# Performance work log

Measured on AMD Instinct MI355X. Metric: run time of the kernel, lower is better.

The kernel has to match this reference:

```python
import jax, jax.numpy as jnp
import numpy as np

N = 100000        # nodes
E = 1600000       # edges (before self-loops)
IN = 128          # in_dim
HID = 16          # hidden_dim per head
HEADS = 8
OUT = 40          # out_dim (classes)
BN_EPS = 1e-5
NEG_SLOPE = 0.2


def setup_inputs() -> dict:
    key = jax.random.key(0)
    ks = jax.random.split(key, 16)
    s = 0.05
    return {
        "x": jax.random.normal(ks[0], (N, IN), dtype=jnp.float32),
        "edge_index": jax.random.randint(ks[1], (2, E), 0, N, dtype=jnp.int64),
        "W1": jax.random.normal(ks[2], (IN, HEADS * HID), dtype=jnp.float32) * s,
        "att_src1": jax.random.normal(ks[3], (HEADS, HID), dtype=jnp.float32) * s,
        "att_dst1": jax.random.normal(ks[4], (HEADS, HID), dtype=jnp.float32) * s,
        "bias1": jax.random.normal(ks[5], (HEADS * HID,), dtype=jnp.float32) * s,
        "bn_gamma": 1.0 + jax.random.normal(ks[6], (HEADS * HID,), dtype=jnp.float32) * 0.1,
        "bn_beta": jax.random.normal(ks[7], (HEADS * HID,), dtype=jnp.float32) * 0.1,
        "bn_mean": jax.random.normal(ks[8], (HEADS * HID,), dtype=jnp.float32) * 0.1,
        "bn_var": jax.random.uniform(ks[9], (HEADS * HID,), dtype=jnp.float32, minval=0.5, maxval=1.5),
        "W2": jax.random.normal(ks[10], (HEADS * HID, OUT), dtype=jnp.float32) * s,
        "att_src2": jax.random.normal(ks[11], (1, OUT), dtype=jnp.float32) * s,
        "att_dst2": jax.random.normal(ks[12], (1, OUT), dtype=jnp.float32) * s,
        "bias2": jax.random.normal(ks[13], (OUT,), dtype=jnp.float32) * s,
        "W_skip": jax.random.normal(ks[14], (IN, HEADS * HID), dtype=jnp.float32) * s,
        "b_skip": jax.random.normal(ks[15], (HEADS * HID,), dtype=jnp.float32) * s,
    }


def gat_conv(x, src, dst, W, a_src, a_dst, bias, heads, ch, concat):
    """PyG GATConv (eval mode): per-edge attention, segment softmax over dst, scatter-add."""
    n = x.shape[0]
    h = (x @ W).reshape(n, heads, ch)                      # [N,H,C]
    alpha_s = jnp.einsum("nhc,hc->nh", h, a_src)            # [N,H]
    alpha_d = jnp.einsum("nhc,hc->nh", h, a_dst)            # [N,H]
    e = jax.nn.leaky_relu(alpha_s[src] + alpha_d[dst], NEG_SLOPE)   # [E,H]
    # numerically stable segment softmax over destination node
    m = jax.ops.segment_max(e, dst, num_segments=n)          # [N,H]
    ex = jnp.exp(e - m[dst])                                 # [E,H]
    denom = jax.ops.segment_sum(ex, dst, num_segments=n)     # [N,H]
    alpha = ex / (denom[dst] + 1e-16)                        # [E,H]
    out = jax.ops.segment_sum(alpha[:, :, None] * h[src], dst, num_segments=n)  # [N,H,C]
    out = out.reshape(n, heads * ch) if concat else out.mean(axis=1)
    return out + bias


def reference(x, edge_index, W1, att_src1, att_dst1, bias1,
              bn_gamma, bn_beta, bn_mean, bn_var,
              W2, att_src2, att_dst2, bias2, W_skip, b_skip):
    n = x.shape[0]
    # add self-loops (PyG GATConv default)
    loops = jnp.arange(n, dtype=edge_index.dtype)
    src = jnp.concatenate([edge_index[0], loops])
    dst = jnp.concatenate([edge_index[1], loops])

    identity = x @ W_skip + b_skip                           # skip projection

    h = gat_conv(x, src, dst, W1, att_src1, att_dst1, bias1, HEADS, HID, True)
    h = (h - bn_mean) * (bn_gamma / jnp.sqrt(bn_var + BN_EPS)) + bn_beta  # BN eval
    h = jax.nn.elu(h)                                        # dropout: eval no-op
    h = h + identity

    att_s2 = att_src2  # [1,OUT] heads=1
    out = gat_conv(h, src, dst, W2, att_s2, att_dst2, bias2, 1, OUT, False)
    return jax.nn.log_softmax(out, axis=1)
```

## Files before the change

kernel.cpp:

```cpp
#include <hip/hip_runtime.h>
#include <math.h>

#define NEG_SLOPE 0.2f
#define BN_EPS 1e-5f
#define BSH 9
#define BMASK 511
#define LOG2E 1.44269504088896f
#define BCAP 12288
#define CH_MAX 3400

typedef __attribute__((ext_vector_type(8))) short short8;
typedef __attribute__((ext_vector_type(4))) float f32x4;
typedef __attribute__((ext_vector_type(2))) float f32x2;

__device__ __forceinline__ float wave_max64(float v) {
  #pragma unroll
  for (int o = 32; o; o >>= 1) v = fmaxf(v, __shfl_xor(v, o, 64));
  return v;
}
__device__ __forceinline__ float wave_sum64(float v) {
  #pragma unroll
  for (int o = 32; o; o >>= 1) v += __shfl_xor(v, o, 64);
  return v;
}

__device__ __forceinline__ unsigned pack2bf(float a, float b) {
  unsigned ua = __float_as_uint(a);
  unsigned ub = __float_as_uint(b);
  ua = ua + 0x7fffu + ((ua >> 16) & 1u);
  ub = ub + 0x7fffu + ((ub >> 16) & 1u);
  return (ua >> 16) | (ub & 0xffff0000u);
}
__device__ __forceinline__ float bf_lo(unsigned u) { return __uint_as_float(u << 16); }
__device__ __forceinline__ float bf_hi(unsigned u) { return __uint_as_float(u & 0xffff0000u); }

union U8 { short8 s; uint4 u; };

__global__ void prep_kernel(const float* __restrict__ W1,
                            const float* __restrict__ att_s,
                            const float* __restrict__ att_d,
                            float* __restrict__ Mext,
                            const float* __restrict__ W2,
                            const float* __restrict__ att_s2,
                            const float* __restrict__ att_d2,
                            float* __restrict__ M2ext,
                            int* __restrict__ bcur, int NB)
{
  int k = threadIdx.x;
  if (k < NB) bcur[k] = 0;
  if (k >= 128) return;
  #pragma unroll
  for (int h = 0; h < 8; ++h) {
    float s = 0.f, d = 0.f;
    #pragma unroll
    for (int c = 0; c < 16; ++c) {
      float w = W1[k * 128 + h * 16 + c];
      s += w * att_s[h * 16 + c];
      d += w * att_d[h * 16 + c];
    }
    Mext[k * 16 + h] = s * LOG2E;
    Mext[k * 16 + 8 + h] = d * LOG2E;
  }
  float s2 = 0.f, d2 = 0.f;
  #pragma unroll
  for (int c = 0; c < 40; ++c) {
    float w = W2[k * 40 + c];
    s2 += w * att_s2[c];
    d2 += w * att_d2[c];
  }
  M2ext[k * 2] = s2 * LOG2E;
  M2ext[k * 2 + 1] = d2 * LOG2E;
}

__global__ __launch_bounds__(256) void gemm1_scatter_kernel(
    const float* __restrict__ X, const float* __restrict__ W1,
    const float* __restrict__ Wsk, const float* __restrict__ bsk,
    const float* __restrict__ Mext,
    unsigned short* __restrict__ h1f8, unsigned* __restrict__ identb,
    float* __restrict__ alpha_s, float* __restrict__ alpha_d, int N,
    const int* __restrict__ esrc, const int* __restrict__ edst,
    int* __restrict__ bcur, unsigned* __restrict__ pkbuf,
    int E, int T, int chunk, int NB, int G1)
{
  __shared__ uint4 Asm4[2048];
  const int t = threadIdx.x;

  if ((int)blockIdx.x >= G1) {
    int* hist  = (int*)Asm4;
    int* lbase = hist + 256;
    int* lcur  = hist + 512;
    unsigned* spk = (unsigned*)(hist + 768);
    unsigned char* sbk = (unsigned char*)(spk + CH_MAX);
    const int bid = (int)blockIdx.x - G1;
    hist[t] = 0;
    __syncthreads();
    int s0 = bid * chunk;
    int s1 = min(s0 + chunk, T);
    for (int i = s0 + t; i < s1; i += 256) {
      int d, s;
      if (i < E) { d = edst[i]; s = esrc[i]; } else { d = s = i - E; }
      int b = d >> BSH;
      int li = i - s0;
      spk[li] = ((unsigned)(d & BMASK) << 17) | (unsigned)s;
      sbk[li] = (unsigned char)b;
      atomicAdd(&hist[b], 1);
    }
    __syncthreads();
    if (t < NB) {
      int h = hist[t];
      lbase[t] = t * BCAP + (h ? atomicAdd(&bcur[t], h) : 0);
      lcur[t] = 0;
    }
    __syncthreads();
    const int cnt2 = s1 - s0;
    for (int li = t; li < cnt2; li += 256) {
      int b = sbk[li];
      int p = lbase[b] + atomicAdd(&lcur[b], 1);
      pkbuf[p] = spk[li];
    }
    return;
  }

  const int l = t & 63, wave = t >> 6;
  const int lx = l & 15, ly = l >> 4;
  const int row0 = blockIdx.x * 128;
  const int wn0 = wave * 64;

  short8 b[4][4];
  short8 b4[4] = {};
  #pragma unroll
  for (int nf = 0; nf < 4; ++nf) {
    int c = wn0 + nf * 16 + lx;
    const float* bp = (c < 128) ? (W1 + c) : (Wsk + c - 128);
    #pragma unroll
    for (int kf = 0; kf < 4; ++kf) {
      int k0 = kf * 32 + ly * 8;
      U8 f;
      f.u.x = pack2bf(bp[(k0 + 0) * 128], bp[(k0 + 1) * 128]);
      f.u.y = pack2bf(bp[(k0 + 2) * 128], bp[(k0 + 3) * 128]);
      f.u.z = pack2bf(bp[(k0 + 4) * 128], bp[(k0 + 5) * 128]);
      f.u.w = pack2bf(bp[(k0 + 6) * 128], bp[(k0 + 7) * 128]);
      b[nf][kf] = f.s;
    }
  }
  if (wave == 0) {
    const float* bp = Mext + lx;
    #pragma unroll
    for (int kf = 0; kf < 4; ++kf) {
      int k0 = kf * 32 + ly * 8;
      U8 f;
      f.u.x = pack2bf(bp[(k0 + 0) * 16], bp[(k0 + 1) * 16]);
      f.u.y = pack2bf(bp[(k0 + 2) * 16], bp[(k0 + 3) * 16]);
      f.u.z = pack2bf(bp[(k0 + 4) * 16], bp[(k0 + 5) * 16]);
      f.u.w = pack2bf(bp[(k0 + 6) * 16], bp[(k0 + 7) * 16]);
      b4[kf] = f.s;
    }
  }

  {
    int rl = t >> 1;
    int half = t & 1;
    int r = row0 + rl;
    const float* xp = X + (size_t)r * 128 + half * 64;
    #pragma unroll
    for (int i = 0; i < 8; ++i) {
      float4 f0 = make_float4(0.f, 0.f, 0.f, 0.f), f1 = f0;
      if (r < N) {
        f0 = *(const float4*)(xp + i * 8);
        f1 = *(const float4*)(xp + i * 8 + 4);
      }
      uint4 u;
      u.x = pack2bf(f0.x, f0.y); u.y = pack2bf(f0.z, f0.w);
      u.z = pack2bf(f1.x, f1.y); u.w = pack2bf(f1.z, f1.w);
      int woff = (rl * 256 + half * 128 + i * 16) ^ ((rl & 7) << 4);
      *(uint4*)((char*)Asm4 + woff) = u;
    }
  }
  __syncthreads();

  float bval[4];
  if (wave >= 2) {
    #pragma unroll
    for (int nf = 0; nf < 4; ++nf) bval[nf] = bsk[(wave - 2) * 64 + nf * 16 + lx];
  }

  for (int mf = 0; mf < 8; ++mf) {
    short8 a[4];
    int rowl = mf * 16 + lx;
    #pragma unroll
    for (int kf = 0; kf < 4; ++kf)
      a[kf] = *(short8*)((char*)Asm4 + ((rowl * 256 + kf * 64 + ly * 16) ^ ((lx & 7) << 4)));

    int rbase = row0 + mf * 16 + ly * 4;

    #pragma unroll
    for (int nf = 0; nf < 4; ++nf) {
      f32x4 acc = {0.f, 0.f, 0.f, 0.f};
      #pragma unroll
      for (int kf = 0; kf < 4; ++kf)
        acc = __builtin_amdgcn_mfma_f32_16x16x32_bf16(a[kf], b[nf][kf], acc, 0, 0, 0);
      if (wave < 2) {
        int c = wn0 + nf * 16 + lx;
        #pragma unroll
        for (int reg = 0; reg < 4; ++reg) {
          float v = acc[reg];
          float vp = __shfl_xor(v, 1, 64);
          int r = rbase + reg;
          if (!(lx & 1) && r < N) {
            int u = __builtin_amdgcn_cvt_pk_fp8_f32(v, vp, 0, false);
            *(unsigned short*)((char*)h1f8 + (unsigned)r * 128u + (unsigned)c) =
                (unsigned short)u;
          }
        }
      } else {
        int c = (wave - 2) * 64 + nf * 16 + lx;
        #pragma unroll
        for (int reg = 0; reg < 4; ++reg) {
          float v = acc[reg] + bval[nf];
          float vp = __shfl_xor(v, 1, 64);
          int r = rbase + reg;
          if (!(lx & 1) && r < N)
            identb[(unsigned)r * 64u + (unsigned)(c >> 1)] = pack2bf(v, vp);
        }
      }
    }

    if (wave == 0) {
      f32x4 acc = {0.f, 0.f, 0.f, 0.f};
      #pragma unroll
      for (int kf = 0; kf < 4; ++kf)
        acc = __builtin_amdgcn_mfma_f32_16x16x32_bf16(a[kf], b4[kf], acc, 0, 0, 0);
      #pragma unroll
      for (int reg = 0; reg < 4; ++reg) {
        int r = rbase + reg;
        if (r < N) {
          if (lx < 8) alpha_s[(size_t)r * 8 + lx] = acc[reg];
          else        alpha_d[(size_t)r * 8 + (lx - 8)] = acc[reg];
        }
      }
    }
  }
}

__global__ __launch_bounds__(256) void passB_kernel(
    const unsigned* __restrict__ pkbuf, const int* __restrict__ bcnt,
    int* __restrict__ starts, int* __restrict__ ends,
    int* __restrict__ ssrc, int N)
{
  __shared__ int cnt[512];
  __shared__ int ps[256];
  __shared__ int cur[512];
  const int t = threadIdx.x;
  const int b = blockIdx.x;
  const int bs = b * BCAP;
  const int be = bs + bcnt[b];

  cnt[t] = 0; cnt[t + 256] = 0;
  __syncthreads();
  for (int i = bs + t; i < be; i += 256)
    atomicAdd(&cnt[pkbuf[i] >> 17], 1);
  __syncthreads();

  int a = cnt[2 * t], b2 = cnt[2 * t + 1];
  ps[t] = a + b2;
  __syncthreads();
  for (int d = 1; d < 256; d <<= 1) {
    int u = (t >= d) ? ps[t - d] : 0;
    __syncthreads();
    ps[t] += u;
    __syncthreads();
  }
  int excl = ps[t] - (a + b2);
  cur[2 * t] = excl;
  cur[2 * t + 1] = excl + a;
  __syncthreads();

  const int node0 = b << BSH;
  {
    int n0 = node0 + 2 * t, n1 = node0 + 2 * t + 1;
    if (n0 < N) { starts[n0] = bs + cur[2 * t];     ends[n0] = bs + cur[2 * t] + a; }
    if (n1 < N) { starts[n1] = bs + cur[2 * t + 1]; ends[n1] = bs + cur[2 * t + 1] + b2; }
  }
  __syncthreads();

  for (int i = bs + t; i < be; i += 256) {
    unsigned pk = pkbuf[i];
    int d = pk >> 17;
    int p = atomicAdd(&cur[d], 1);
    ssrc[bs + p] = (int)(pk & 0x1FFFFu);
  }
}

__global__ __launch_bounds__(256) void agg1_kernel(
    const int* __restrict__ starts, const int* __restrict__ ends,
    const int* __restrict__ ssrc,
    const float* __restrict__ as1, const float* __restrict__ ad1,
    const unsigned short* __restrict__ h1f8,
    const float* __restrict__ bias1, const float* __restrict__ gamma,
    const float* __restrict__ beta, const float* __restrict__ mean,
    const float* __restrict__ var,
    const unsigned* __restrict__ identb, unsigned* __restrict__ hpostb, int N)
{
  const int w = threadIdx.x >> 6, l = threadIdx.x & 63;
  const int n = blockIdx.x * 4 + w;
  if (n >= N) return;
  const int e8 = l & 7;
  const int hh = l >> 3;
  const int hb4 = (l & 56) << 2;
  const int c0 = l * 2;
  const unsigned l2 = (unsigned)(l * 2);
  const float adp = ad1[(unsigned)n * 8u + (unsigned)hh];
  const int jb = starts[n], je = ends[n];

  const float bb0 = bias1[c0], bb1 = bias1[c0 + 1];
  const float sc0 = gamma[c0] * rsqrtf(var[c0] + BN_EPS);
  const float sc1 = gamma[c0 + 1] * rsqrtf(var[c0 + 1] + BN_EPS);
  const float mn0 = mean[c0], mn1 = mean[c0 + 1];
  const float bt0 = beta[c0], bt1 = beta[c0 + 1];

  const char* h1c = (const char*)h1f8;

  float dsum = 0.f;
  f32x2 acc2 = {0.f, 0.f};

#define PHASE2(K, SVEC, EW) { \
    unsigned sk = (unsigned)__builtin_amdgcn_readlane(SVEC, (K)); \
    float ewk = __uint_as_float((unsigned) \
        __builtin_amdgcn_ds_swizzle((int)__float_as_uint(EW), 0x18 | ((K) << 5))); \
    unsigned u8 = *(const unsigned short*)(h1c + ((size_t)sk << 7) + l2); \
    f32x2 hv = __builtin_amdgcn_cvt_pk_f32_fp8((int)u8, false); \
    acc2 += ewk * hv; }

  int j = jb;
  for (; j + 8 <= je; j += 8) {
    int svec = ssrc[j + e8];
    float e = as1[(unsigned)svec * 8u + (unsigned)hh] + adp;
    e = fmaxf(e, NEG_SLOPE * e);
    float ew = exp2f(e);
    dsum += ew;
    PHASE2(0, svec, ew) PHASE2(1, svec, ew) PHASE2(2, svec, ew) PHASE2(3, svec, ew)
    PHASE2(4, svec, ew) PHASE2(5, svec, ew) PHASE2(6, svec, ew) PHASE2(7, svec, ew)
  }
  int rem = je - j;
  if (rem > 0) {
    int jj = j + (e8 < rem ? e8 : 0);
    int svec = ssrc[jj];
    float e = as1[(unsigned)svec * 8u + (unsigned)hh] + adp;
    e = fmaxf(e, NEG_SLOPE * e);
    float ew = (e8 < rem) ? exp2f(e) : 0.f;
    dsum += ew;
    for (int k = 0; k < rem; ++k) {
      unsigned sk = (unsigned)__builtin_amdgcn_readlane(svec, k);
      float ewk = __uint_as_float(
          __builtin_amdgcn_ds_bpermute(hb4 + (k << 2), __float_as_uint(ew)));
      unsigned u8 = *(const unsigned short*)(h1c + ((size_t)sk << 7) + l2);
      f32x2 hv = __builtin_amdgcn_cvt_pk_f32_fp8((int)u8, false);
      acc2 += ewk * hv;
    }
  }
#undef PHASE2

  dsum += __shfl_xor(dsum, 1, 64);
  dsum += __shfl_xor(dsum, 2, 64);
  dsum += __shfl_xor(dsum, 4, 64);

  float inv = 1.f / (dsum + 1e-16f);
  unsigned uid = identb[(unsigned)n * 64u + (unsigned)l];
  float o0 = acc2.x * inv + bb0;
  float o1 = acc2.y * inv + bb1;
  o0 = (o0 - mn0) * sc0 + bt0;
  o1 = (o1 - mn1) * sc1 + bt1;
  o0 = o0 > 0.f ? o0 : expm1f(o0);
  o1 = o1 > 0.f ? o1 : expm1f(o1);
  o0 += bf_lo(uid); o1 += bf_hi(uid);
  hpostb[(unsigned)n * 64u + (unsigned)l] = pack2bf(o0, o1);
}

__global__ __launch_bounds__(256) void gemm2_kernel(
    const unsigned* __restrict__ hpostb, const float* __restrict__ W2,
    const float* __restrict__ M2ext,
    unsigned* __restrict__ h2a8, unsigned* __restrict__ h2b28,
    float* __restrict__ as2, float* __restrict__ ad2, int N)
{
  const int t = threadIdx.x;
  const int l = t & 63, wave = t >> 6;
  const int lx = l & 15, ly = l >> 4;
  const int row0 = blockIdx.x * 128;

  short8 b[3][4];
  short8 b4[4];
  {
    #pragma unroll
    for (int nf = 0; nf < 3; ++nf) {
      int col = nf * 16 + lx;
      bool v = col < 40;
      const float* bp = W2 + (v ? col : 0);
      #pragma unroll
      for (int kf = 0; kf < 4; ++kf) {
        int k0 = kf * 32 + ly * 8;
        U8 f;
        if (v) {
          f.u.x = pack2bf(bp[(k0 + 0) * 40], bp[(k0 + 1) * 40]);
          f.u.y = pack2bf(bp[(k0 + 2) * 40], bp[(k0 + 3) * 40]);
          f.u.z = pack2bf(bp[(k0 + 4) * 40], bp[(k0 + 5) * 40]);
          f.u.w = pack2bf(bp[(k0 + 6) * 40], bp[(k0 + 7) * 40]);
        } else {
          f.u = make_uint4(0, 0, 0, 0);
        }
        b[nf][kf] = f.s;
      }
    }
    bool va = lx < 2;
    const float* bp = M2ext + (va ? lx : 0);
    #pragma unroll
    for (int kf = 0; kf < 4; ++kf) {
      int k0 = kf * 32 + ly * 8;
      U8 f;
      if (va) {
        f.u.x = pack2bf(bp[(k0 + 0) * 2], bp[(k0 + 1) * 2]);
        f.u.y = pack2bf(bp[(k0 + 2) * 2], bp[(k0 + 3) * 2]);
        f.u.z = pack2bf(bp[(k0 + 4) * 2], bp[(k0 + 5) * 2]);
        f.u.w = pack2bf(bp[(k0 + 6) * 2], bp[(k0 + 7) * 2]);
      } else {
        f.u = make_uint4(0, 0, 0, 0);
      }
      b4[kf] = f.s;
    }
  }

  #pragma unroll
  for (int i2 = 0; i2 < 2; ++i2) {
    int mf = wave * 2 + i2;
    int arow = row0 + mf * 16 + lx;
    short8 a[4];
    #pragma unroll
    for (int kf = 0; kf < 4; ++kf) {
      U8 f;
      f.u = make_uint4(0, 0, 0, 0);
      if (arow < N)
        f.u = *(const uint4*)(hpostb + (unsigned)arow * 64u + (unsigned)(kf * 16 + ly * 4));
      a[kf] = f.s;
    }

    int rbase = row0 + mf * 16 + ly * 4;

    #pragma unroll
    for (int nf = 0; nf < 3; ++nf) {
      f32x4 acc = {0.f, 0.f, 0.f, 0.f};
      #pragma unroll
      for (int kf = 0; kf < 4; ++kf)
        acc = __builtin_amdgcn_mfma_f32_16x16x32_bf16(a[kf], b[nf][kf], acc, 0, 0, 0);
      int c = nf * 16 + lx;
      #pragma unroll
      for (int reg = 0; reg < 4; ++reg) {
        float v = acc[reg];
        float v1 = __shfl_xor(v, 1, 64);
        float v2 = __shfl_xor(v, 2, 64);
        float v3 = __shfl_xor(v1, 2, 64);
        int r = rbase + reg;
        if (r < N && c < 40 && !(lx & 3)) {
          int u = __builtin_amdgcn_cvt_pk_fp8_f32(v, v1, 0, false);
          u = __builtin_amdgcn_cvt_pk_fp8_f32(v2, v3, u, true);
          int c4 = c >> 2;
          if (c < 32) h2a8[((unsigned)r << 3) + (unsigned)c4] = (unsigned)u;
          else        h2b28[((unsigned)r << 1) + (unsigned)(c4 - 8)] = (unsigned)u;
        }
      }
    }
    {
      f32x4 acc = {0.f, 0.f, 0.f, 0.f};
      #pragma unroll
      for (int kf = 0; kf < 4; ++kf)
        acc = __builtin_amdgcn_mfma_f32_16x16x32_bf16(a[kf], b4[kf], acc, 0, 0, 0);
      #pragma unroll
      for (int reg = 0; reg < 4; ++reg) {
        int r = rbase + reg;
        if (r < N) {
          if (lx == 0) as2[r] = acc[reg];
          else if (lx == 1) ad2[r] = acc[reg];
        }
      }
    }
  }
}

__global__ __launch_bounds__(256) void agg2_kernel(
    const int* __restrict__ starts, const int* __restrict__ ends,
    const int* __restrict__ ssrc,
    const float* __restrict__ as2, const float* __restrict__ ad2,
    const unsigned* __restrict__ h2a8, const unsigned* __restrict__ h2b28,
    const float* __restrict__ bias2,
    float* __restrict__ outp, int N)
{
  const int w = threadIdx.x >> 6, l = threadIdx.x & 63;
  const int n = blockIdx.x * 4 + w;
  if (n >= N) return;
  const int g = l / 10;
  const int q = l - g * 10;
  const bool act = l < 60;
  const float ad = ad2[n];
  const int jb = starts[n], je = ends[n];

  const char* hbase = (q < 8) ? ((const char*)h2a8 + (unsigned)q * 4u)
                              : ((const char*)h2b28 + (unsigned)(q - 8) * 4u);
  const unsigned hshift = (q < 8) ? 5u : 3u;
  const char* as2c = (const char*)as2;

  float dsum = 0.f;
  f32x2 acc01 = {0.f, 0.f}, acc23 = {0.f, 0.f};

#define EDGE2(JJ, GUARD) { \
    bool v_ = act && (GUARD); \
    unsigned s = v_ ? (unsigned)ssrc[JJ] : 0u; \
    float e = *(const float*)(as2c + (s << 2)) + ad; \
    e = fmaxf(e, NEG_SLOPE * e); \
    float ex = v_ ? exp2f(e) : 0.f; \
    unsigned u = *(const unsigned*)(hbase + ((size_t)s << hshift)); \
    dsum += ex; \
    f32x2 lo = __builtin_amdgcn_cvt_pk_f32_fp8((int)u, false); \
    f32x2 hi = __builtin_amdgcn_cvt_pk_f32_fp8((int)u, true); \
    acc01 += ex * lo; \
    acc23 += ex * hi; }

  int j = jb;
  for (; j + 12 <= je; j += 12) {
    EDGE2(j + g, true)
    EDGE2(j + 6 + g, true)
  }
  for (; j < je; j += 6) {
    EDGE2(j + g, (j + g) < je)
  }
#undef EDGE2

  float a0 = acc01.x, a1 = acc01.y, a2 = acc23.x, a3 = acc23.y;

#define COMB(A) { \
    float t_ = A + __shfl(A, l + 30, 64); \
    A = t_ + __shfl(t_, l + 10, 64) + __shfl(t_, l + 20, 64); }
  COMB(a0) COMB(a1) COMB(a2) COMB(a3) COMB(dsum)
#undef COMB

  float inv = 1.f / (dsum + 1e-16f);
  float o0 = a0 * inv + bias2[q * 4 + 0];
  float o1 = a1 * inv + bias2[q * 4 + 1];
  float o2 = a2 * inv + bias2[q * 4 + 2];
  float o3 = a3 * inv + bias2[q * 4 + 3];

  float m4 = fmaxf(fmaxf(o0, o1), fmaxf(o2, o3));
  float mx = wave_max64(l < 10 ? m4 : -3.4e38f);
  float se = wave_sum64(l < 10 ? __expf(o0 - mx) + __expf(o1 - mx) +
                                 __expf(o2 - mx) + __expf(o3 - mx) : 0.f);
  float ls = logf(se);
  if (l < 10)
    *(float4*)&outp[(size_t)n * 40 + q * 4] =
        make_float4(o0 - mx - ls, o1 - mx - ls, o2 - mx - ls, o3 - mx - ls);
}

extern "C" void kernel_launch(void* const* d_in, const int* in_sizes, int n_in,
                              void* d_out, int out_size, void* d_ws, size_t ws_size,
                              hipStream_t stream)
{
  const float* x        = (const float*)d_in[0];
  const int*   ei       = (const int*)d_in[1];
  const float* W1       = (const float*)d_in[2];
  const float* att_src1 = (const float*)d_in[3];
  const float* att_dst1 = (const float*)d_in[4];
  const float* bias1    = (const float*)d_in[5];
  const float* bn_gamma = (const float*)d_in[6];
  const float* bn_beta  = (const float*)d_in[7];
  const float* bn_mean  = (const float*)d_in[8];
  const float* bn_var   = (const float*)d_in[9];
  const float* W2       = (const float*)d_in[10];
  const float* att_src2 = (const float*)d_in[11];
  const float* att_dst2 = (const float*)d_in[12];
  const float* bias2    = (const float*)d_in[13];
  const float* W_skip   = (const float*)d_in[14];
  const float* b_skip   = (const float*)d_in[15];

  const int N = in_sizes[0] / 128;
  const int E = in_sizes[1] / 2;
  const int T = E + N;
  const int NB = (N + BMASK) >> BSH;

  char* p = (char*)d_ws;
  auto alloc = [&](size_t bytes) { char* q = p; p += (bytes + 255) & ~255ull; return q; };
  unsigned short* h1f8 = (unsigned short*)alloc((size_t)N * 128);
  unsigned* hpostb = (unsigned*)alloc((size_t)N * 64 * 4);
  unsigned* identb = (unsigned*)alloc((size_t)N * 64 * 4);
  float* as1     = (float*)alloc((size_t)N * 8 * 4);
  float* ad1     = (float*)alloc((size_t)N * 8 * 4);
  float* Mext    = (float*)alloc(128 * 16 * 4);
  float* M2ext   = (float*)alloc(128 * 2 * 4);
  int*   starts  = (int*)alloc((size_t)N * 4);
  int*   ends    = (int*)alloc((size_t)N * 4);
  unsigned* pkbuf= (unsigned*)alloc((size_t)NB * BCAP * 4);
  int*   ssrc    = (int*)alloc((size_t)NB * BCAP * 4);
  int*   bcur    = (int*)alloc((size_t)NB * 4);
  unsigned* h2a8  = (unsigned*)h1f8;
  unsigned* h2b28 = (unsigned*)((char*)h1f8 + (size_t)N * 32);
  float* as2 = as1;
  float* ad2 = ad1;

  const int* ei_src = ei;
  const int* ei_dst = ei + E;

  prep_kernel<<<1, 256, 0, stream>>>(W1, att_src1, att_dst1, Mext,
                                     W2, att_src2, att_dst2, M2ext,
                                     bcur, NB);

  const int G1 = (N + 127) / 128;
  int NBLK_A = (T + CH_MAX - 1) / CH_MAX;
  if (NBLK_A < 512) NBLK_A = 512;
  const int chunk = (T + NBLK_A - 1) / NBLK_A;
  gemm1_scatter_kernel<<<G1 + NBLK_A, 256, 0, stream>>>(
      x, W1, W_skip, b_skip, Mext, h1f8, identb, as1, ad1, N,
      ei_src, ei_dst, bcur, pkbuf, E, T, chunk, NB, G1);

  passB_kernel<<<NB, 256, 0, stream>>>(pkbuf, bcur, starts, ends, ssrc, N);

  agg1_kernel<<<(N + 3) / 4, 256, 0, stream>>>(starts, ends, ssrc, as1, ad1, h1f8,
                                               bias1, bn_gamma, bn_beta, bn_mean, bn_var,
                                               identb, hpostb, N);
  gemm2_kernel<<<(N + 127) / 128, 256, 0, stream>>>(hpostb, W2, M2ext,
                                                    h2a8, h2b28, as2, ad2, N);
  agg2_kernel<<<(N + 3) / 4, 256, 0, stream>>>(starts, ends, ssrc, as2, ad2,
                                               h2a8, h2b28, bias2,
                                               (float*)d_out, N);
}
```

Before: 230.3 us.

## Prepack bf16 weight fragments in prep kernel and store skip projection as fp8

The prep kernel now runs on four blocks and packs W1/W_skip, the attention projection matrices and W2 into bf16 column-major buffers. The GEMM kernels can then load MFMA B fragments with single 16-byte loads instead of strided fp32 gathers and per-block conversion. The skip projection identity is also stored as fp8 instead of bf16, which halves its write and read traffic between gemm1 and agg1. The cost is lower precision on the residual term.

```diff
diff --git a/kernel.cpp b/kernel.cpp
--- a/kernel.cpp
+++ b/kernel.cpp
@@ -36,47 +36,87 @@
 
 union U8 { short8 s; uint4 u; };
 
-__global__ void prep_kernel(const float* __restrict__ W1,
-                            const float* __restrict__ att_s,
-                            const float* __restrict__ att_d,
-                            float* __restrict__ Mext,
-                            const float* __restrict__ W2,
-                            const float* __restrict__ att_s2,
-                            const float* __restrict__ att_d2,
-                            float* __restrict__ M2ext,
-                            int* __restrict__ bcur, int NB)
+__global__ __launch_bounds__(256) void prep_kernel(
+    const float* __restrict__ W1, const float* __restrict__ Wsk,
+    const float* __restrict__ att_s, const float* __restrict__ att_d,
+    const float* __restrict__ W2,
+    const float* __restrict__ att_s2, const float* __restrict__ att_d2,
+    unsigned short* __restrict__ Bbuf, unsigned short* __restrict__ Mextbuf,
+    unsigned short* __restrict__ B2buf,
+    int* __restrict__ bcur, int NB)
 {
-  int k = threadIdx.x;
-  if (k < NB) bcur[k] = 0;
-  if (k >= 128) return;
-  #pragma unroll
-  for (int h = 0; h < 8; ++h) {
-    float s = 0.f, d = 0.f;
-    #pragma unroll
-    for (int c = 0; c < 16; ++c) {
-      float w = W1[k * 128 + h * 16 + c];
-      s += w * att_s[h * 16 + c];
-      d += w * att_d[h * 16 + c];
-    }
-    Mext[k * 16 + h] = s * LOG2E;
-    Mext[k * 16 + 8 + h] = d * LOG2E;
-  }
-  float s2 = 0.f, d2 = 0.f;
-  #pragma unroll
-  for (int c = 0; c < 40; ++c) {
-    float w = W2[k * 40 + c];
-    s2 += w * att_s2[c];
-    d2 += w * att_d2[c];
-  }
-  M2ext[k * 2] = s2 * LOG2E;
-  M2ext[k * 2 + 1] = d2 * LOG2E;
+  const int t = threadIdx.x;
+  const int bid = blockIdx.x;
+
+  if (bid == 0) {
+    __shared__ float Ms[128][16];
+    __shared__ float M2s[128][2];
+    if (t < NB) bcur[t] = 0;
+    if (t < 128) {
+      int k = t;
+      #pragma unroll
+      for (int h = 0; h < 8; ++h) {
+        float s = 0.f, d = 0.f;
+        #pragma unroll
+        for (int c = 0; c < 16; ++c) {
+          float w = W1[k * 128 + h * 16 + c];
+          s += w * att_s[h * 16 + c];
+          d += w * att_d[h * 16 + c];
+        }
+        Ms[k][h] = s * LOG2E;
+        Ms[k][8 + h] = d * LOG2E;
+      }
+      float s2 = 0.f, d2 = 0.f;
+      #pragma unroll
+      for (int c = 0; c < 40; ++c) {
+        float w = W2[k * 40 + c];
+        s2 += w * att_s2[c];
+        d2 += w * att_d2[c];
+      }
+      M2s[k][0] = s2 * LOG2E;
+      M2s[k][1] = d2 * LOG2E;
+    }
+    __syncthreads();
+    unsigned* Mu = (unsigned*)Mextbuf;
+    for (int idx = t; idx < 16 * 64; idx += 256) {
+      int h = idx >> 6, u = idx & 63;
+      Mu[h * 64 + u] = pack2bf(Ms[2 * u][h], Ms[2 * u + 1][h]);
+    }
+    unsigned* B2u = (unsigned*)B2buf;
+    for (int idx = t; idx < 2 * 64; idx += 256) {
+      int cc = idx >> 6, u = idx & 63;
+      B2u[(48 + cc) * 64 + u] = pack2bf(M2s[2 * u][cc], M2s[2 * u + 1][cc]);
+    }
+  } else if (bid <= 2) {
+    int c = (bid - 1) * 128 + (t >> 1);
+    int half = t & 1;
+    const float* src = (c < 128) ? (W1 + c) : (Wsk + (c - 128));
+    unsigned* out = (unsigned*)Bbuf + c * 64 + half * 32;
+    #pragma unroll 8
+    for (int u = 0; u < 32; ++u) {
+      int k = half * 64 + 2 * u;
+      out[u] = pack2bf(src[(size_t)k * 128], src[(size_t)(k + 1) * 128]);
+    }
+  } else {
+    unsigned* B2u = (unsigned*)B2buf;
+    for (int idx = t; idx < 40 * 64; idx += 256) {
+      int c = idx >> 6, u = idx & 63;
+      B2u[c * 64 + u] = pack2bf(W2[(2 * u) * 40 + c], W2[(2 * u + 1) * 40 + c]);
+    }
+    for (int idx = t; idx < 22 * 64; idx += 256) {
+      int zc = idx >> 6, u = idx & 63;
+      int c = (zc < 8) ? (40 + zc) : (50 + (zc - 8));
+      B2u[c * 64 + u] = 0;
+    }
+  }
 }
 
 __global__ __launch_bounds__(256) void gemm1_scatter_kernel(
-    const float* __restrict__ X, const float* __restrict__ W1,
-    const float* __restrict__ Wsk, const float* __restrict__ bsk,
-    const float* __restrict__ Mext,
-    unsigned short* __restrict__ h1f8, unsigned* __restrict__ identb,
+    const float* __restrict__ X,
+    const unsigned short* __restrict__ Bbuf,
+    const unsigned short* __restrict__ Mextbuf,
+    const float* __restrict__ bsk,
+    unsigned short* __restrict__ h1f8, unsigned short* __restrict__ identf8,
     float* __restrict__ alpha_s, float* __restrict__ alpha_d, int N,
     const int* __restrict__ esrc, const int* __restrict__ edst,
     int* __restrict__ bcur, unsigned* __restrict__ pkbuf,
@@ -131,30 +171,14 @@
   #pragma unroll
   for (int nf = 0; nf < 4; ++nf) {
     int c = wn0 + nf * 16 + lx;
-    const float* bp = (c < 128) ? (W1 + c) : (Wsk + c - 128);
-    #pragma unroll
-    for (int kf = 0; kf < 4; ++kf) {
-      int k0 = kf * 32 + ly * 8;
-      U8 f;
-      f.u.x = pack2bf(bp[(k0 + 0) * 128], bp[(k0 + 1) * 128]);
-      f.u.y = pack2bf(bp[(k0 + 2) * 128], bp[(k0 + 3) * 128]);
-      f.u.z = pack2bf(bp[(k0 + 4) * 128], bp[(k0 + 5) * 128]);
-      f.u.w = pack2bf(bp[(k0 + 6) * 128], bp[(k0 + 7) * 128]);
-      b[nf][kf] = f.s;
-    }
+    #pragma unroll
+    for (int kf = 0; kf < 4; ++kf)
+      b[nf][kf] = *(const short8*)(Bbuf + c * 128 + kf * 32 + ly * 8);
   }
   if (wave == 0) {
-    const float* bp = Mext + lx;
-    #pragma unroll
-    for (int kf = 0; kf < 4; ++kf) {
-      int k0 = kf * 32 + ly * 8;
-      U8 f;
-      f.u.x = pack2bf(bp[(k0 + 0) * 16], bp[(k0 + 1) * 16]);
-      f.u.y = pack2bf(bp[(k0 + 2) * 16], bp[(k0 + 3) * 16]);
-      f.u.z = pack2bf(bp[(k0 + 4) * 16], bp[(k0 + 5) * 16]);
-      f.u.w = pack2bf(bp[(k0 + 6) * 16], bp[(k0 + 7) * 16]);
-      b4[kf] = f.s;
-    }
+    #pragma unroll
+    for (int kf = 0; kf < 4; ++kf)
+      b4[kf] = *(const short8*)(Mextbuf + lx * 128 + kf * 32 + ly * 8);
   }
 
   {
@@ -219,8 +243,11 @@
           float v = acc[reg] + bval[nf];
           float vp = __shfl_xor(v, 1, 64);
           int r = rbase + reg;
-          if (!(lx & 1) && r < N)
-            identb[(unsigned)r * 64u + (unsigned)(c >> 1)] = pack2bf(v, vp);
+          if (!(lx & 1) && r < N) {
+            int u = __builtin_amdgcn_cvt_pk_fp8_f32(v, vp, 0, false);
+            *(unsigned short*)((char*)identf8 + (unsigned)r * 128u + (unsigned)c) =
+                (unsigned short)u;
+          }
         }
       }
     }
@@ -299,7 +326,7 @@
     const float* __restrict__ bias1, const float* __restrict__ gamma,
     const float* __restrict__ beta, const float* __restrict__ mean,
     const float* __restrict__ var,
-    const unsigned* __restrict__ identb, unsigned* __restrict__ hpostb, int N)
+    const unsigned short* __restrict__ identf8, unsigned* __restrict__ hpostb, int N)
 {
   const int w = threadIdx.x >> 6, l = threadIdx.x & 63;
   const int n = blockIdx.x * 4 + w;
@@ -365,20 +392,20 @@
   dsum += __shfl_xor(dsum, 4, 64);
 
   float inv = 1.f / (dsum + 1e-16f);
-  unsigned uid = identb[(unsigned)n * 64u + (unsigned)l];
+  unsigned uid8 = *(const unsigned short*)((const char*)identf8 + ((unsigned)n << 7) + l2);
+  f32x2 idv = __builtin_amdgcn_cvt_pk_f32_fp8((int)uid8, false);
   float o0 = acc2.x * inv + bb0;
   float o1 = acc2.y * inv + bb1;
   o0 = (o0 - mn0) * sc0 + bt0;
   o1 = (o1 - mn1) * sc1 + bt1;
   o0 = o0 > 0.f ? o0 : expm1f(o0);
   o1 = o1 > 0.f ? o1 : expm1f(o1);
-  o0 += bf_lo(uid); o1 += bf_hi(uid);
+  o0 += idv.x; o1 += idv.y;
   hpostb[(unsigned)n * 64u + (unsigned)l] = pack2bf(o0, o1);
 }
 
 __global__ __launch_bounds__(256) void gemm2_kernel(
-    const unsigned* __restrict__ hpostb, const float* __restrict__ W2,
-    const float* __restrict__ M2ext,
+    const unsigned* __restrict__ hpostb, const unsigned short* __restrict__ B2buf,
     unsigned* __restrict__ h2a8, unsigned* __restrict__ h2b28,
     float* __restrict__ as2, float* __restrict__ ad2, int N)
 {
@@ -389,44 +416,16 @@
 
   short8 b[3][4];
   short8 b4[4];
-  {
-    #pragma unroll
-    for (int nf = 0; nf < 3; ++nf) {
-      int col = nf * 16 + lx;
-      bool v = col < 40;
-      const float* bp = W2 + (v ? col : 0);
-      #pragma unroll
-      for (int kf = 0; kf < 4; ++kf) {
-        int k0 = kf * 32 + ly * 8;
-        U8 f;
-        if (v) {
-          f.u.x = pack2bf(bp[(k0 + 0) * 40], bp[(k0 + 1) * 40]);
-          f.u.y = pack2bf(bp[(k0 + 2) * 40], bp[(k0 + 3) * 40]);
-          f.u.z = pack2bf(bp[(k0 + 4) * 40], bp[(k0 + 5) * 40]);
-          f.u.w = pack2bf(bp[(k0 + 6) * 40], bp[(k0 + 7) * 40]);
-        } else {
-          f.u = make_uint4(0, 0, 0, 0);
-        }
-        b[nf][kf] = f.s;
-      }
-    }
-    bool va = lx < 2;
-    const float* bp = M2ext + (va ? lx : 0);
-    #pragma unroll
-    for (int kf = 0; kf < 4; ++kf) {
-      int k0 = kf * 32 + ly * 8;
-      U8 f;
-      if (va) {
-        f.u.x = pack2bf(bp[(k0 + 0) * 2], bp[(k0 + 1) * 2]);
-        f.u.y = pack2bf(bp[(k0 + 2) * 2], bp[(k0 + 3) * 2]);
-        f.u.z = pack2bf(bp[(k0 + 4) * 2], bp[(k0 + 5) * 2]);
-        f.u.w = pack2bf(bp[(k0 + 6) * 2], bp[(k0 + 7) * 2]);
-      } else {
-        f.u = make_uint4(0, 0, 0, 0);
-      }
-      b4[kf] = f.s;
-    }
-  }
+  #pragma unroll
+  for (int nf = 0; nf < 3; ++nf) {
+    int c = nf * 16 + lx;
+    #pragma unroll
+    for (int kf = 0; kf < 4; ++kf)
+      b[nf][kf] = *(const short8*)(B2buf + c * 128 + kf * 32 + ly * 8);
+  }
+  #pragma unroll
+  for (int kf = 0; kf < 4; ++kf)
+    b4[kf] = *(const short8*)(B2buf + (48 + lx) * 128 + kf * 32 + ly * 8);
 
   #pragma unroll
   for (int i2 = 0; i2 < 2; ++i2) {
@@ -584,13 +583,14 @@
 
   char* p = (char*)d_ws;
   auto alloc = [&](size_t bytes) { char* q = p; p += (bytes + 255) & ~255ull; return q; };
-  unsigned short* h1f8 = (unsigned short*)alloc((size_t)N * 128);
+  unsigned short* h1f8   = (unsigned short*)alloc((size_t)N * 128);
+  unsigned short* identf8= (unsigned short*)alloc((size_t)N * 128);
   unsigned* hpostb = (unsigned*)alloc((size_t)N * 64 * 4);
-  unsigned* identb = (unsigned*)alloc((size_t)N * 64 * 4);
   float* as1     = (float*)alloc((size_t)N * 8 * 4);
   float* ad1     = (float*)alloc((size_t)N * 8 * 4);
-  float* Mext    = (float*)alloc(128 * 16 * 4);
-  float* M2ext   = (float*)alloc(128 * 2 * 4);
+  unsigned short* Bbuf   = (unsigned short*)alloc(256 * 128 * 2);
+  unsigned short* Mextbuf= (unsigned short*)alloc(16 * 128 * 2);
+  unsigned short* B2buf  = (unsigned short*)alloc(64 * 128 * 2);
   int*   starts  = (int*)alloc((size_t)N * 4);
   int*   ends    = (int*)alloc((size_t)N * 4);
   unsigned* pkbuf= (unsigned*)alloc((size_t)NB * BCAP * 4);
@@ -604,24 +604,24 @@
   const int* ei_src = ei;
   const int* ei_dst = ei + E;
 
-  prep_kernel<<<1, 256, 0, stream>>>(W1, att_src1, att_dst1, Mext,
-                                     W2, att_src2, att_dst2, M2ext,
-                                     bcur, NB);
+  prep_kernel<<<4, 256, 0, stream>>>(W1, W_skip, att_src1, att_dst1,
+                                     W2, att_src2, att_dst2,
+                                     Bbuf, Mextbuf, B2buf, bcur, NB);
 
   const int G1 = (N + 127) / 128;
   int NBLK_A = (T + CH_MAX - 1) / CH_MAX;
   if (NBLK_A < 512) NBLK_A = 512;
   const int chunk = (T + NBLK_A - 1) / NBLK_A;
   gemm1_scatter_kernel<<<G1 + NBLK_A, 256, 0, stream>>>(
-      x, W1, W_skip, b_skip, Mext, h1f8, identb, as1, ad1, N,
+      x, Bbuf, Mextbuf, b_skip, h1f8, identf8, as1, ad1, N,
       ei_src, ei_dst, bcur, pkbuf, E, T, chunk, NB, G1);
 
   passB_kernel<<<NB, 256, 0, stream>>>(pkbuf, bcur, starts, ends, ssrc, N);
 
   agg1_kernel<<<(N + 3) / 4, 256, 0, stream>>>(starts, ends, ssrc, as1, ad1, h1f8,
                                                bias1, bn_gamma, bn_beta, bn_mean, bn_var,
-                                               identb, hpostb, N);
-  gemm2_kernel<<<(N + 127) / 128, 256, 0, stream>>>(hpostb, W2, M2ext,
+                                               identf8, hpostb, N);
+  gemm2_kernel<<<(N + 127) / 128, 256, 0, stream>>>(hpostb, B2buf,
                                                     h2a8, h2b28, as2, ad2, N);
   agg2_kernel<<<(N + 3) / 4, 256, 0, stream>>>(starts, ends, ssrc, as2, ad2,
                                                h2a8, h2b28, bias2,
```

Result: faster. 222.4 us (-3.4%).
